# Performance work log

Measured on AMD Instinct MI355X. Metric: run time of the kernel, lower is better.

Reference implementation:

```python
import jax, jax.numpy as jnp
import numpy as np

H_DIM = 1024
NUM_HEADS = 16
HEAD_DIM = H_DIM // NUM_HEADS
EPS = 1e-5


def rms_norm(x, w, eps=EPS):
    var = jnp.mean(jnp.square(x), axis=-1, keepdims=True)
    return x * jax.lax.rsqrt(var + eps) * w


def setup_inputs() -> dict:
    key = jax.random.key(0)
    ks = jax.random.split(key, 8)
    B, S = 2, 2048
    x = jax.random.normal(ks[0], (B, S, H_DIM), dtype=jnp.float32)
    # learned params (orthogonal init approximated by scaled normal for a correctness baseline)
    qkv_w = jax.random.normal(ks[1], (3 * H_DIM, H_DIM), dtype=jnp.float32) / np.sqrt(H_DIM)
    gate_w = jax.random.normal(ks[2], (NUM_HEADS, H_DIM), dtype=jnp.float32) / np.sqrt(H_DIM)
    o_w = jax.random.normal(ks[3], (H_DIM, H_DIM), dtype=jnp.float32) / np.sqrt(H_DIM)
    prenorm_w = jnp.ones((H_DIM,), dtype=jnp.float32)
    q_norm_w = jnp.ones((HEAD_DIM,), dtype=jnp.float32)
    k_norm_w = jnp.ones((HEAD_DIM,), dtype=jnp.float32)
    return {"x": x, "prenorm_w": prenorm_w, "qkv_w": qkv_w, "gate_w": gate_w,
            "o_w": o_w, "q_norm_w": q_norm_w, "k_norm_w": k_norm_w}


def reference(x, prenorm_w, qkv_w, gate_w, o_w, q_norm_w, k_norm_w):
    B, S, D = x.shape
    residual = x
    xn = rms_norm(x, prenorm_w)                                   # [B,S,D]
    qkv = jnp.einsum('bsd,ed->bse', xn, qkv_w)                    # [B,S,3D]
    qkv = qkv.reshape(B, S, 3, NUM_HEADS, HEAD_DIM)
    gate = jnp.einsum('bsd,hd->bsh', xn, gate_w)                  # [B,S,H]
    q, k, v = qkv[:, :, 0], qkv[:, :, 1], qkv[:, :, 2]            # [B,S,H,hd]
    q = rms_norm(q, q_norm_w)
    k = rms_norm(k, k_norm_w)
    scale = 1.0 / np.sqrt(HEAD_DIM).astype(np.float32)
    scores = jnp.einsum('bqhd,bkhd->bhqk', q, k) * scale          # [B,H,S,S]
    attn = jax.nn.softmax(scores, axis=-1)
    out = jnp.einsum('bhqk,bkhd->bhqd', attn, v)                  # [B,H,S,hd]
    out = out * jax.nn.sigmoid(gate).transpose(0, 2, 1)[..., None]
    out = out.transpose(0, 2, 1, 3).reshape(B, S, D)              # [B,S,D]
    return jnp.einsum('bsd,ed->bse', out, o_w) + residual
```

## Files before the change

kernel.cpp:

```cpp
#include <hip/hip_runtime.h>
#include <math.h>

typedef __bf16 bf16x8 __attribute__((ext_vector_type(8)));
typedef float f32x4 __attribute__((ext_vector_type(4)));
typedef float f32x16 __attribute__((ext_vector_type(16)));
typedef unsigned int uint2v __attribute__((ext_vector_type(2)));
typedef unsigned int uint4v __attribute__((ext_vector_type(4)));
typedef unsigned short ushort_t;

#define SEQ 2048
#define MROWS 4096
#define EPS 1e-5f
#define QKS 3200
#define LOG2E 1.4426950408889634f
#define SMAX_B2 17.32f

#if __has_builtin(__builtin_amdgcn_exp2f)
#define EXP2(x) __builtin_amdgcn_exp2f(x)
#else
#define EXP2(x) exp2f(x)
#endif

__device__ __forceinline__ float bf2f(ushort_t u) {
  union { unsigned int i; float f; } c; c.i = ((unsigned int)u) << 16; return c.f;
}
__device__ __forceinline__ ushort_t f2bf(float f) {
  union { unsigned int i; float f; } c; c.f = f;
  unsigned int i = c.i;
  unsigned int r = i + 0x7fffu + ((i >> 16) & 1u);
  return (ushort_t)(r >> 16);
}
__device__ __forceinline__ ushort_t f2bf_fast(float f) {
  union { __bf16 b; ushort_t u; } cv; cv.b = (__bf16)f; return cv.u;
}

#define CVTPK(d, a, b) asm("v_cvt_pk_bf16_f32 %0, %1, %2" : "=v"(d) : "v"(a), "v"(b))

__device__ __forceinline__ void plane_swap(unsigned int &a, unsigned int &b) {
#if __has_builtin(__builtin_amdgcn_permlane32_swap)
  uint2v r = __builtin_amdgcn_permlane32_swap(a, b, 0, 0);
  a = r.x; b = r.y;
#else
  unsigned int sa = (unsigned int)__shfl_xor((int)a, 32);
  unsigned int sb = (unsigned int)__shfl_xor((int)b, 32);
  int hi = (int)((threadIdx.x & 63) >> 5);
  unsigned int na = hi ? sb : a;
  unsigned int nb = hi ? b : sa;
  a = na; b = nb;
#endif
}

__device__ __forceinline__ void softmax_pack(const f32x16 &stv, float &lp,
                                             uint4v &Fa, uint4v &Fb) {
  float p[16];
  #pragma unroll
  for (int r = 0; r < 16; ++r) {
    p[r] = EXP2(stv[r] - SMAX_B2);
    lp += p[r];
  }
  unsigned int X00, X01, X10, X11, X20, X21, X30, X31;
  CVTPK(X00, p[0], p[1]);   CVTPK(X01, p[2], p[3]);
  CVTPK(X10, p[4], p[5]);   CVTPK(X11, p[6], p[7]);
  CVTPK(X20, p[8], p[9]);   CVTPK(X21, p[10], p[11]);
  CVTPK(X30, p[12], p[13]); CVTPK(X31, p[14], p[15]);
  plane_swap(X00, X10); plane_swap(X01, X11);
  plane_swap(X20, X30); plane_swap(X21, X31);
  Fa.x = X00; Fa.y = X01; Fa.z = X10; Fa.w = X11;
  Fb.x = X20; Fb.y = X21; Fb.z = X30; Fb.w = X31;
}

__device__ __forceinline__ float wave_sum(float v) {
  #pragma unroll
  for (int off = 32; off > 0; off >>= 1) v += __shfl_xor(v, off);
  return v;
}

__global__ void detect_kernel(const unsigned int* __restrict__ xraw, int* __restrict__ flag) {
  int tid = threadIdx.x;
  int cnt = 0;
  for (int i = tid; i < 4096; i += 256) {
    unsigned int e = (xraw[i] >> 7) & 0xFFu;
    cnt += (e >= 100u && e <= 150u) ? 1 : 0;
  }
  __shared__ int sred[256];
  sred[tid] = cnt;
  __syncthreads();
  for (int s = 128; s > 0; s >>= 1) {
    if (tid < s) sred[tid] += sred[tid + s];
    __syncthreads();
  }
  if (tid == 0) flag[0] = (sred[0] > 2048) ? 1 : 0;
}

__global__ void prep_kernel(const void* __restrict__ qkvw_in, const void* __restrict__ gw_in,
                            const void* __restrict__ ow_in, const void* __restrict__ pw_in,
                            const void* __restrict__ qn_in, const void* __restrict__ kn_in,
                            ushort_t* __restrict__ Wcat, ushort_t* __restrict__ ow,
                            float* __restrict__ pwf, float* __restrict__ qnf,
                            float* __restrict__ knf, const int* __restrict__ flag) {
  int bid = blockIdx.x, tid = threadIdx.x;
  int bf = *flag;
  if (bid < 12288) {
    int i = bid * 256 + tid;
    Wcat[i] = bf ? ((const ushort_t*)qkvw_in)[i] : f2bf(((const float*)qkvw_in)[i]);
  } else if (bid < 12352) {
    int i = (bid - 12288) * 256 + tid;
    Wcat[3072 * 1024 + i] = bf ? ((const ushort_t*)gw_in)[i] : f2bf(((const float*)gw_in)[i]);
  } else if (bid < 16448) {
    int i = (bid - 12352) * 256 + tid;
    ow[i] = bf ? ((const ushort_t*)ow_in)[i] : f2bf(((const float*)ow_in)[i]);
  } else {
    for (int i = tid; i < 1024; i += 256)
      pwf[i] = bf ? bf2f(((const ushort_t*)pw_in)[i]) : ((const float*)pw_in)[i];
    if (tid < 64) {
      qnf[tid] = bf ? bf2f(((const ushort_t*)qn_in)[tid]) : ((const float*)qn_in)[tid];
      knf[tid] = bf ? bf2f(((const ushort_t*)kn_in)[tid]) : ((const float*)kn_in)[tid];
    }
  }
}

__global__ void prenorm_kernel(const void* __restrict__ xraw,
                               const float* __restrict__ w,
                               ushort_t* __restrict__ xn,
                               const int* __restrict__ flag) {
  int row = blockIdx.x;
  int tid = threadIdx.x;
  float4 u;
  if (*flag) {
    ushort4 s = ((const ushort4*)xraw)[row * 256 + tid];
    u.x = bf2f(s.x); u.y = bf2f(s.y); u.z = bf2f(s.z); u.w = bf2f(s.w);
  } else {
    u = ((const float4*)xraw)[row * 256 + tid];
  }
  float ss = u.x*u.x + u.y*u.y + u.z*u.z + u.w*u.w;
  ss = wave_sum(ss);
  __shared__ float red[4];
  if ((tid & 63) == 0) red[tid >> 6] = ss;
  __syncthreads();
  float total = red[0] + red[1] + red[2] + red[3];
  float inv = rsqrtf(total * (1.0f / 1024.0f) + EPS);
  float4 wu = ((const float4*)w)[tid];
  ushort4 o;
  o.x = f2bf(u.x * inv * wu.x);
  o.y = f2bf(u.y * inv * wu.y);
  o.z = f2bf(u.z * inv * wu.z);
  o.w = f2bf(u.w * inv * wu.w);
  ((ushort4*)(xn + (long long)row * 1024))[tid] = o;
}

__device__ __forceinline__ void gll16(const ushort_t* g, ushort_t* l) {
  __builtin_amdgcn_global_load_lds(
      (const __attribute__((address_space(1))) unsigned int*)g,
      (__attribute__((address_space(3))) unsigned int*)l, 16, 0, 0);
}

__global__ void gemm_qkv_fused(const ushort_t* __restrict__ A, const ushort_t* __restrict__ B,
                               ushort_t* __restrict__ C, float* __restrict__ gate,
                               const float* __restrict__ qw, const float* __restrict__ kw) {
  __shared__ ushort_t As[128 * 32];
  __shared__ ushort_t Bs[128 * 32];
  int tid = threadIdx.x, wave = tid >> 6, lane = tid & 63;
  int m_blk = blockIdx.y * 128, n_blk = blockIdx.x * 128;
  int wm = (wave & 1) * 64, wn = (wave >> 1) * 64;
  int g = lane >> 4, c = lane & 15;
  int arow = lane >> 2;
  int akc = (lane & 3) << 3;
  f32x4 acc[4][4] = {};
  for (int kt = 0; kt < 1024; kt += 32) {
    #pragma unroll
    for (int i = 0; i < 2; ++i) {
      int rbase = (i * 4 + wave) * 16;
      gll16(A + (long long)(m_blk + rbase + arow) * 1024 + kt + akc, &As[rbase * 32]);
      gll16(B + (long long)(n_blk + rbase + arow) * 1024 + kt + akc, &Bs[rbase * 32]);
    }
    __syncthreads();
    bf16x8 af[4], bfr[4];
    #pragma unroll
    for (int mi = 0; mi < 4; ++mi)
      af[mi] = *(const bf16x8*)&As[(wm + mi * 16 + c) * 32 + (g << 3)];
    #pragma unroll
    for (int ni = 0; ni < 4; ++ni)
      bfr[ni] = *(const bf16x8*)&Bs[(wn + ni * 16 + c) * 32 + (g << 3)];
    #pragma unroll
    for (int mi = 0; mi < 4; ++mi)
      #pragma unroll
      for (int ni = 0; ni < 4; ++ni)
        acc[mi][ni] = __builtin_amdgcn_mfma_f32_16x16x32_bf16(af[mi], bfr[ni], acc[mi][ni], 0, 0, 0);
    __syncthreads();
  }
  int col_base = n_blk + wn;
  if (col_base < 2048) {
    int isk = col_base >= 1024;
    float scale = isk ? 1.0f : (0.125f * LOG2E);
    const float* nw = isk ? kw : qw;
    float w[4];
    #pragma unroll
    for (int ni = 0; ni < 4; ++ni) w[ni] = nw[ni * 16 + c];
    #pragma unroll
    for (int mi = 0; mi < 4; ++mi)
      #pragma unroll
      for (int r = 0; r < 4; ++r) {
        float ss = 0.f;
        #pragma unroll
        for (int ni = 0; ni < 4; ++ni) ss += acc[mi][ni][r] * acc[mi][ni][r];
        #pragma unroll
        for (int off = 8; off > 0; off >>= 1) ss += __shfl_xor(ss, off);
        float inv = rsqrtf(ss * (1.0f / 64.0f) + EPS) * scale;
        int row = m_blk + wm + mi * 16 + g * 4 + r;
        #pragma unroll
        for (int ni = 0; ni < 4; ++ni)
          C[(long long)row * QKS + col_base + ni * 16 + c] = f2bf(acc[mi][ni][r] * inv * w[ni]);
      }
  } else if (col_base < 3072) {
    #pragma unroll
    for (int mi = 0; mi < 4; ++mi)
      #pragma unroll
      for (int r = 0; r < 4; ++r) {
        int row = m_blk + wm + mi * 16 + g * 4 + r;
        #pragma unroll
        for (int ni = 0; ni < 4; ++ni)
          C[(long long)row * QKS + col_base + ni * 16 + c] = f2bf(acc[mi][ni][r]);
      }
  } else if (col_base == 3072) {
    #pragma unroll
    for (int mi = 0; mi < 4; ++mi)
      #pragma unroll
      for (int r = 0; r < 4; ++r) {
        int row = m_blk + wm + mi * 16 + g * 4 + r;
        float v = acc[mi][0][r];
        gate[(long long)row * 16 + c] = 1.0f / (1.0f + __expf(-v));
      }
  }
}

__global__ void gemm_tiled(const ushort_t* __restrict__ A, const ushort_t* __restrict__ B,
                           void* __restrict__ Cv, const void* __restrict__ res,
                           const int* __restrict__ flag,
                           int K, int lda, int ldb, int ldc) {
  __shared__ ushort_t As[128 * 32];
  __shared__ ushort_t Bs[128 * 32];
  int tid = threadIdx.x, wave = tid >> 6, lane = tid & 63;
  int m_blk = blockIdx.y * 128, n_blk = blockIdx.x * 128;
  int wm = (wave & 1) * 64, wn = (wave >> 1) * 64;
  int g = lane >> 4, c = lane & 15;
  int arow = lane >> 2;
  int akc = (lane & 3) << 3;
  f32x4 acc[4][4] = {};
  for (int kt = 0; kt < K; kt += 32) {
    #pragma unroll
    for (int i = 0; i < 2; ++i) {
      int rbase = (i * 4 + wave) * 16;
      gll16(A + (long long)(m_blk + rbase + arow) * lda + kt + akc, &As[rbase * 32]);
      gll16(B + (long long)(n_blk + rbase + arow) * ldb + kt + akc, &Bs[rbase * 32]);
    }
    __syncthreads();
    bf16x8 af[4], bfr[4];
    #pragma unroll
    for (int mi = 0; mi < 4; ++mi)
      af[mi] = *(const bf16x8*)&As[(wm + mi * 16 + c) * 32 + (g << 3)];
    #pragma unroll
    for (int ni = 0; ni < 4; ++ni)
      bfr[ni] = *(const bf16x8*)&Bs[(wn + ni * 16 + c) * 32 + (g << 3)];
    #pragma unroll
    for (int mi = 0; mi < 4; ++mi)
      #pragma unroll
      for (int ni = 0; ni < 4; ++ni)
        acc[mi][ni] = __builtin_amdgcn_mfma_f32_16x16x32_bf16(af[mi], bfr[ni], acc[mi][ni], 0, 0, 0);
    __syncthreads();
  }
  int outbf = flag ? *flag : 1;
  #pragma unroll
  for (int mi = 0; mi < 4; ++mi)
    #pragma unroll
    for (int ni = 0; ni < 4; ++ni)
      #pragma unroll
      for (int r = 0; r < 4; ++r) {
        int row = m_blk + wm + mi * 16 + g * 4 + r;
        int col = n_blk + wn + ni * 16 + c;
        long long idx = (long long)row * ldc + col;
        float v = acc[mi][ni][r];
        if (res) v += outbf ? bf2f(((const ushort_t*)res)[idx]) : ((const float*)res)[idx];
        if (outbf) ((ushort_t*)Cv)[idx] = f2bf(v);
        else       ((float*)Cv)[idx] = v;
      }
}

__global__ void vt_kernel(const ushort_t* __restrict__ qkv, ushort_t* __restrict__ Vt) {
  __shared__ ushort_t tile[64][65];
  int s0 = blockIdx.x * 64;
  int bh = blockIdx.y;
  int b = bh >> 4, h = bh & 15;
  const ushort_t* src = qkv + (long long)b * SEQ * QKS + 2048 + h * 64;
  int d = threadIdx.x & 63, srow = threadIdx.x >> 6;
  #pragma unroll
  for (int i = 0; i < 16; ++i) {
    int sl = i * 4 + srow;
    tile[sl][d] = src[(long long)(s0 + sl) * QKS + d];
  }
  __syncthreads();
  ushort_t* dst = Vt + (long long)bh * 64 * SEQ + s0;
  int sl2 = threadIdx.x & 63, drow = threadIdx.x >> 6;
  #pragma unroll
  for (int i = 0; i < 16; ++i) {
    int dd = i * 4 + drow;
    dst[(long long)dd * SEQ + sl2] = tile[sl2][dd];
  }
}

__global__ void flash_kernel(const ushort_t* __restrict__ qkv, const ushort_t* __restrict__ Vt,
                             const float* __restrict__ gate, ushort_t* __restrict__ ao) {
  __shared__ ushort_t Ks[2][64 * 64];
  __shared__ ushort_t Vs[2][64 * 64];
  int tid = threadIdx.x, wave = tid >> 6, lane = tid & 63;
  int al = lane & 31, hi = lane >> 5;
  int q0 = blockIdx.x * 128;
  int bh = blockIdx.y, b = bh >> 4, h = bh & 15;
  const ushort_t* qbase = qkv + (long long)b * SEQ * QKS + h * 64;
  const ushort_t* kbase = qbase + 1024;
  const ushort_t* vtbase = Vt + (long long)bh * 64 * SEQ;
  int qrow = q0 + wave * 32 + al;
  bf16x8 bq[4];
  #pragma unroll
  for (int dst = 0; dst < 4; ++dst)
    bq[dst] = *(const bf16x8*)(qbase + (long long)qrow * QKS + dst * 16 + hi * 8);
  f32x16 oac0 = {}, oac1 = {};
  float lp = 0.f;
  int srow = lane >> 3;
  int schk = lane & 7;

  #define STAGE(BUF, S0) do {                                                        \
    _Pragma("unroll")                                                                \
    for (int t = 0; t < 2; ++t) {                                                    \
      int rb = t * 32 + wave * 8;                                                    \
      int row = rb + srow;                                                           \
      int gch = (schk ^ (row & 7)) << 3;                                             \
      gll16(kbase + (long long)((S0) + row) * QKS + gch, &Ks[BUF][rb * 64]);         \
      gll16(vtbase + (long long)row * SEQ + (S0) + gch, &Vs[BUF][rb * 64]);          \
    } } while (0)

  #define COMPUTE(BUF) do {                                                          \
    f32x16 st0 = {}, st1 = {};                                                       \
    __builtin_amdgcn_s_setprio(1);                                                   \
    _Pragma("unroll")                                                                \
    for (int dst = 0; dst < 4; ++dst) {                                              \
      int ph = (((dst << 1) | hi) ^ (al & 7)) << 3;                                  \
      bf16x8 ak0 = *(const bf16x8*)&Ks[BUF][al * 64 + ph];                           \
      bf16x8 ak1 = *(const bf16x8*)&Ks[BUF][(32 + al) * 64 + ph];                    \
      st0 = __builtin_amdgcn_mfma_f32_32x32x16_bf16(ak0, bq[dst], st0, 0, 0, 0);     \
      st1 = __builtin_amdgcn_mfma_f32_32x32x16_bf16(ak1, bq[dst], st1, 0, 0, 0);     \
    }                                                                                \
    __builtin_amdgcn_s_setprio(0);                                                   \
    uint4v Fa, Fb, Fc, Fd;                                                           \
    softmax_pack(st0, lp, Fa, Fb);                                                   \
    softmax_pack(st1, lp, Fc, Fd);                                                   \
    bf16x8 pf0 = __builtin_bit_cast(bf16x8, Fa);                                     \
    bf16x8 pf1 = __builtin_bit_cast(bf16x8, Fb);                                     \
    bf16x8 pf2 = __builtin_bit_cast(bf16x8, Fc);                                     \
    bf16x8 pf3 = __builtin_bit_cast(bf16x8, Fd);                                     \
    __builtin_amdgcn_s_setprio(1);                                                   \
    _Pragma("unroll")                                                                \
    for (int kst = 0; kst < 4; ++kst) {                                              \
      int ph = (((kst << 1) | hi) ^ (al & 7)) << 3;                                  \
      bf16x8 av0 = *(const bf16x8*)&Vs[BUF][al * 64 + ph];                           \
      bf16x8 av1 = *(const bf16x8*)&Vs[BUF][(32 + al) * 64 + ph];                    \
      bf16x8 pf = (kst == 0) ? pf0 : (kst == 1) ? pf1 : (kst == 2) ? pf2 : pf3;      \
      oac0 = __builtin_amdgcn_mfma_f32_32x32x16_bf16(av0, pf, oac0, 0, 0, 0);        \
      oac1 = __builtin_amdgcn_mfma_f32_32x32x16_bf16(av1, pf, oac1, 0, 0, 0);        \
    }                                                                                \
    __builtin_amdgcn_s_setprio(0);                                                   \
  } while (0)

  STAGE(0, 0);
  __syncthreads();
  for (int s0 = 0; s0 < SEQ; s0 += 128) {
    STAGE(1, s0 + 64);
    COMPUTE(0);
    __syncthreads();
    if (s0 + 128 < SEQ) STAGE(0, s0 + 128);
    COMPUTE(1);
    __syncthreads();
  }
  #undef STAGE
  #undef COMPUTE

  float ltot = lp + __shfl_xor(lp, 32);
  float sg = gate[(long long)(b * SEQ + qrow) * 16 + h];
  float scale = sg / ltot;
  ushort_t* aobase = ao + (long long)(b * SEQ + qrow) * 1024 + h * 64;
  #define OSTORE(OA, MT) do {                                                        \
    _Pragma("unroll")                                                                \
    for (int t = 0; t < 4; ++t) {                                                    \
      ushort4 o;                                                                     \
      o.x = f2bf_fast(OA[4 * t + 0] * scale);                                        \
      o.y = f2bf_fast(OA[4 * t + 1] * scale);                                        \
      o.z = f2bf_fast(OA[4 * t + 2] * scale);                                        \
      o.w = f2bf_fast(OA[4 * t + 3] * scale);                                        \
      *(ushort4*)(aobase + (MT) * 32 + 8 * t + 4 * hi) = o;                          \
    } } while (0)
  OSTORE(oac0, 0);
  OSTORE(oac1, 1);
  #undef OSTORE
}

extern "C" void kernel_launch(void* const* d_in, const int* in_sizes, int n_in,
                              void* d_out, int out_size, void* d_ws, size_t ws_size,
                              hipStream_t stream) {
  (void)in_sizes; (void)n_in; (void)out_size; (void)ws_size;
  char* ws = (char*)d_ws;
  ushort_t* Wcat = (ushort_t*)(ws);
  ushort_t* ow   = (ushort_t*)(ws + (7ll << 20));
  float*    pwf  = (float*)   (ws + (9ll << 20));
  float*    qnf  = (float*)   (ws + (9ll << 20) + (8 << 10));
  float*    knf  = (float*)   (ws + (9ll << 20) + (12 << 10));
  int*      flag = (int*)     (ws + (9ll << 20) + (16 << 10));
  float*    gate = (float*)   (ws + (9ll << 20) + (64 << 10));
  ushort_t* xn   = (ushort_t*)(ws + (10ll << 20));
  ushort_t* qkv2 = (ushort_t*)(ws + (18ll << 20));
  ushort_t* Vt   = (ushort_t*)(ws + (44ll << 20));
  ushort_t* ao   = (ushort_t*)(ws + (52ll << 20));

  detect_kernel<<<1, 256, 0, stream>>>((const unsigned int*)d_in[0], flag);
  prep_kernel<<<16449, 256, 0, stream>>>(d_in[2], d_in[3], d_in[4], d_in[1], d_in[5], d_in[6],
                                         Wcat, ow, pwf, qnf, knf, flag);
  prenorm_kernel<<<MROWS, 256, 0, stream>>>(d_in[0], pwf, xn, flag);
  gemm_qkv_fused<<<dim3(25, 32), 256, 0, stream>>>(xn, Wcat, qkv2, gate, qnf, knf);
  vt_kernel<<<dim3(32, 32), 256, 0, stream>>>(qkv2, Vt);
  flash_kernel<<<dim3(16, 32), 256, 0, stream>>>(qkv2, Vt, gate, ao);
  gemm_tiled<<<dim3(8, 32), 256, 0, stream>>>(ao, ow, d_out, d_in[0], flag,
                                              1024, 1024, 1024, 1024);
}
```

Measured before the change: 233.9 us.

## Deepen flash attention K/V pipeline to four LDS buffers with vmcnt barriers

Moves the flash kernel from a double-buffered K/V staging loop with full __syncthreads to a four-buffer ring that prefetches two tiles ahead. It waits with explicit s_waitcnt vmcnt counts plus s_barrier, so only the oldest loads must land before compute. It also changes the LDS XOR swizzle to mix in bits 3-4 of the row, aimed at fewer bank conflicts. The softmax exp uses raw v_exp_f32 with a tree-reduced row sum. LDS use doubles, which may lower occupancy, and the hand-counted vmcnt values must match the number of loads issued per stage.

```diff
diff --git a/kernel.cpp b/kernel.cpp
--- a/kernel.cpp
+++ b/kernel.cpp
@@ -15,12 +15,6 @@
 #define LOG2E 1.4426950408889634f
 #define SMAX_B2 17.32f
 
-#if __has_builtin(__builtin_amdgcn_exp2f)
-#define EXP2(x) __builtin_amdgcn_exp2f(x)
-#else
-#define EXP2(x) exp2f(x)
-#endif
-
 __device__ __forceinline__ float bf2f(ushort_t u) {
   union { unsigned int i; float f; } c; c.i = ((unsigned int)u) << 16; return c.f;
 }
@@ -32,6 +26,10 @@
 }
 __device__ __forceinline__ ushort_t f2bf_fast(float f) {
   union { __bf16 b; ushort_t u; } cv; cv.b = (__bf16)f; return cv.u;
+}
+
+__device__ __forceinline__ float exp2_raw(float x) {
+  float r; asm("v_exp_f32 %0, %1" : "=v"(r) : "v"(x)); return r;
 }
 
 #define CVTPK(d, a, b) asm("v_cvt_pk_bf16_f32 %0, %1, %2" : "=v"(d) : "v"(a), "v"(b))
@@ -54,10 +52,12 @@
                                              uint4v &Fa, uint4v &Fb) {
   float p[16];
   #pragma unroll
-  for (int r = 0; r < 16; ++r) {
-    p[r] = EXP2(stv[r] - SMAX_B2);
-    lp += p[r];
-  }
+  for (int r = 0; r < 16; ++r) p[r] = exp2_raw(stv[r] - SMAX_B2);
+  float s0 = (p[0] + p[1]) + (p[2] + p[3]);
+  float s1 = (p[4] + p[5]) + (p[6] + p[7]);
+  float s2 = (p[8] + p[9]) + (p[10] + p[11]);
+  float s3 = (p[12] + p[13]) + (p[14] + p[15]);
+  lp += (s0 + s1) + (s2 + s3);
   unsigned int X00, X01, X10, X11, X20, X21, X30, X31;
   CVTPK(X00, p[0], p[1]);   CVTPK(X01, p[2], p[3]);
   CVTPK(X10, p[4], p[5]);   CVTPK(X11, p[6], p[7]);
@@ -309,10 +309,11 @@
 
 __global__ void flash_kernel(const ushort_t* __restrict__ qkv, const ushort_t* __restrict__ Vt,
                              const float* __restrict__ gate, ushort_t* __restrict__ ao) {
-  __shared__ ushort_t Ks[2][64 * 64];
-  __shared__ ushort_t Vs[2][64 * 64];
+  __shared__ ushort_t Ks[4][64 * 64];
+  __shared__ ushort_t Vs[4][64 * 64];
   int tid = threadIdx.x, wave = tid >> 6, lane = tid & 63;
   int al = lane & 31, hi = lane >> 5;
+  int fal = (al & 7) ^ ((al >> 3) & 3);
   int q0 = blockIdx.x * 128;
   int bh = blockIdx.y, b = bh >> 4, h = bh & 15;
   const ushort_t* qbase = qkv + (long long)b * SEQ * QKS + h * 64;
@@ -329,21 +330,27 @@
   int schk = lane & 7;
 
   #define STAGE(BUF, S0) do {                                                        \
+    int gch = ((schk ^ srow ^ wave) & 7) << 3;                                       \
     _Pragma("unroll")                                                                \
-    for (int t = 0; t < 2; ++t) {                                                    \
-      int rb = t * 32 + wave * 8;                                                    \
+    for (int tt = 0; tt < 2; ++tt) {                                                 \
+      int rb = tt * 32 + wave * 8;                                                   \
       int row = rb + srow;                                                           \
-      int gch = (schk ^ (row & 7)) << 3;                                             \
       gll16(kbase + (long long)((S0) + row) * QKS + gch, &Ks[BUF][rb * 64]);         \
       gll16(vtbase + (long long)row * SEQ + (S0) + gch, &Vs[BUF][rb * 64]);          \
     } } while (0)
+
+  #define PIPE_BAR(N) do {                                                           \
+    asm volatile("s_waitcnt vmcnt(" #N ")" ::: "memory");                            \
+    __builtin_amdgcn_s_barrier();                                                    \
+    asm volatile("" ::: "memory");                                                   \
+  } while (0)
 
   #define COMPUTE(BUF) do {                                                          \
     f32x16 st0 = {}, st1 = {};                                                       \
     __builtin_amdgcn_s_setprio(1);                                                   \
     _Pragma("unroll")                                                                \
     for (int dst = 0; dst < 4; ++dst) {                                              \
-      int ph = (((dst << 1) | hi) ^ (al & 7)) << 3;                                  \
+      int ph = (((dst << 1) | hi) ^ fal) << 3;                                       \
       bf16x8 ak0 = *(const bf16x8*)&Ks[BUF][al * 64 + ph];                           \
       bf16x8 ak1 = *(const bf16x8*)&Ks[BUF][(32 + al) * 64 + ph];                    \
       st0 = __builtin_amdgcn_mfma_f32_32x32x16_bf16(ak0, bq[dst], st0, 0, 0, 0);     \
@@ -360,7 +367,7 @@
     __builtin_amdgcn_s_setprio(1);                                                   \
     _Pragma("unroll")                                                                \
     for (int kst = 0; kst < 4; ++kst) {                                              \
-      int ph = (((kst << 1) | hi) ^ (al & 7)) << 3;                                  \
+      int ph = (((kst << 1) | hi) ^ fal) << 3;                                       \
       bf16x8 av0 = *(const bf16x8*)&Vs[BUF][al * 64 + ph];                           \
       bf16x8 av1 = *(const bf16x8*)&Vs[BUF][(32 + al) * 64 + ph];                    \
       bf16x8 pf = (kst == 0) ? pf0 : (kst == 1) ? pf1 : (kst == 2) ? pf2 : pf3;      \
@@ -371,16 +378,18 @@
   } while (0)
 
   STAGE(0, 0);
-  __syncthreads();
-  for (int s0 = 0; s0 < SEQ; s0 += 128) {
-    STAGE(1, s0 + 64);
-    COMPUTE(0);
-    __syncthreads();
-    if (s0 + 128 < SEQ) STAGE(0, s0 + 128);
-    COMPUTE(1);
-    __syncthreads();
-  }
+  STAGE(1, 64);
+  for (int it = 0; it < 30; ++it) {
+    STAGE((it + 2) & 3, (it + 2) * 64);
+    PIPE_BAR(8);
+    COMPUTE(it & 3);
+  }
+  PIPE_BAR(4);
+  COMPUTE(2);
+  PIPE_BAR(0);
+  COMPUTE(3);
   #undef STAGE
+  #undef PIPE_BAR
   #undef COMPUTE
 
   float ltot = lp + __shfl_xor(lp, 32);
@@ -389,13 +398,13 @@
   ushort_t* aobase = ao + (long long)(b * SEQ + qrow) * 1024 + h * 64;
   #define OSTORE(OA, MT) do {                                                        \
     _Pragma("unroll")                                                                \
-    for (int t = 0; t < 4; ++t) {                                                    \
+    for (int tt = 0; tt < 4; ++tt) {                                                 \
       ushort4 o;                                                                     \
-      o.x = f2bf_fast(OA[4 * t + 0] * scale);                                        \
-      o.y = f2bf_fast(OA[4 * t + 1] * scale);                                        \
-      o.z = f2bf_fast(OA[4 * t + 2] * scale);                                        \
-      o.w = f2bf_fast(OA[4 * t + 3] * scale);                                        \
-      *(ushort4*)(aobase + (MT) * 32 + 8 * t + 4 * hi) = o;                          \
+      o.x = f2bf_fast(OA[4 * tt + 0] * scale);                                       \
+      o.y = f2bf_fast(OA[4 * tt + 1] * scale);                                       \
+      o.z = f2bf_fast(OA[4 * tt + 2] * scale);                                       \
+      o.w = f2bf_fast(OA[4 * tt + 3] * scale);                                       \
+      *(ushort4*)(aobase + (MT) * 32 + 8 * tt + 4 * hi) = o;                         \
     } } while (0)
   OSTORE(oac0, 0);
   OSTORE(oac1, 1);
```

New measurement: 230.4 us. No clear change (-1.5%).
